# Kernel tuning notes

Hardware: AMD Instinct MI355X
Metric: run time of the kernel (lower is better)

The kernel has to match this reference:

```python
import jax, jax.numpy as jnp
import numpy as np

N = 8192
IN_C = 512
OUT_C = 512


def setup_inputs() -> dict:
    key = jax.random.key(0)
    k1, k2, k3 = jax.random.split(key, 3)
    x = jax.random.normal(k1, (N, IN_C), dtype=jnp.float32)
    adj = jax.random.uniform(k2, (N, N), dtype=jnp.float32)
    # torch.rand initializer for the weight (uniform [0,1))
    w = jax.random.uniform(k3, (IN_C, OUT_C), dtype=jnp.float32)
    return {"x": x, "adj": adj, "w": w}


def reference(x, adj, w):
    # A = adj + I
    A = adj + jnp.eye(adj.shape[0], dtype=adj.dtype)
    # D_hat = diag(deg)^{-1/2}; diagonal inverse + sqrt == elementwise rsqrt of degrees
    deg = jnp.sum(A, axis=1)                      # [N]
    d_inv_sqrt = jax.lax.rsqrt(deg)               # [N]
    # A_hat = D_hat @ A @ D_hat == row/col scaling (same math, no dense inverse)
    A_hat = A * d_inv_sqrt[:, None] * d_inv_sqrt[None, :]
    mm_1 = A_hat @ x                              # [N, in_c]
    return jax.nn.elu(mm_1 @ w)                   # [N, out_c]
```

## Files before the change

### kernel.cpp

```cpp
#include <hip/hip_runtime.h>

#define NN 8192
#define CC 512

typedef __attribute__((ext_vector_type(8))) short short8;
typedef __attribute__((ext_vector_type(4))) float f32x4;
typedef unsigned short ushort_t;

__device__ __forceinline__ unsigned short f2bf(float f) {
    unsigned int u = __float_as_uint(f);
    u += 0x7FFF + ((u >> 16) & 1);
    return (unsigned short)(u >> 16);
}
__device__ __forceinline__ float bf2f(unsigned short u) {
    return __uint_as_float(((unsigned int)u) << 16);
}

__device__ __forceinline__ void gload_lds16(const void* g, void* l) {
    __builtin_amdgcn_global_load_lds((const __attribute__((address_space(1))) unsigned int*)g,
                                     (__attribute__((address_space(3))) unsigned int*)l,
                                     16, 0, 0);
}

__global__ __launch_bounds__(256) void k_pre(const float* __restrict__ x,
                                             const float* __restrict__ adj,
                                             const ushort_t* __restrict__ wt,
                                             float* __restrict__ ds,
                                             ushort_t* __restrict__ adj16,
                                             float* __restrict__ z) {
    __shared__ __align__(16) ushort_t As[128 * 64];
    __shared__ __align__(16) ushort_t Bs[128 * 64];
    __shared__ float partial[4];

    int t = threadIdx.x;
    if (blockIdx.x >= 256) {
        int row = blockIdx.x - 256;
        const float4* p = (const float4*)(adj + (size_t)row * NN);
        ushort4* q = (ushort4*)(adj16 + (size_t)row * NN);
        float s = 0.f;
#pragma unroll
        for (int i = 0; i < 8; ++i) {
            float4 v = p[t + i * 256];
            s += (v.x + v.y) + (v.z + v.w);
            ushort4 u;
            u.x = f2bf(v.x); u.y = f2bf(v.y); u.z = f2bf(v.z); u.w = f2bf(v.w);
            q[t + i * 256] = u;
        }
#pragma unroll
        for (int off = 32; off > 0; off >>= 1) s += __shfl_down(s, off, 64);
        if ((t & 63) == 0) partial[t >> 6] = s;
        __syncthreads();
        if (t == 0) {
            float deg = ((partial[0] + partial[1]) + (partial[2] + partial[3])) + 1.0f;
            ds[row] = rsqrtf(deg);
        }
        return;
    }

    int bid = blockIdx.x;
    int wid = t >> 6, lane = t & 63;
    int cb = bid & 3, rb = bid >> 2;
    int rowBase = rb * 128, colBase = cb * 128;

    int ar = t >> 4, ac4 = t & 15;
    const float* aptr = x + (size_t)(rowBase + ar) * CC + ac4 * 4;
    int srow0 = t >> 3, ss = t & 7;

    f32x4 acc[4][4] = {};
    int wr = wid >> 1, wc = wid & 1;
    int fr = lane & 15, fq = lane >> 4;

    for (int kt = 0; kt < CC / 64; ++kt) {
#pragma unroll
        for (int i2 = 0; i2 < 8; ++i2) {
            float4 v = *(const float4*)(aptr + kt * 64 + (size_t)i2 * 16 * CC);
            int row = i2 * 16 + ar;
            ushort4 u2;
            u2.x = f2bf(v.x); u2.y = f2bf(v.y); u2.z = f2bf(v.z); u2.w = f2bf(v.w);
            *(ushort4*)((char*)As + row * 128 + ((ac4 * 8) ^ ((row & 7) << 4))) = u2;
        }
#pragma unroll
        for (int j = 0; j < 4; ++j) {
            int row = j * 32 + srow0;
            gload_lds16((const char*)(wt + (size_t)(colBase + row) * CC + kt * 64 +
                                      ((ss ^ (row & 7)) << 3)),
                        (char*)Bs + j * 4096 + wid * 1024);
        }
        __syncthreads();
#pragma unroll
        for (int ks = 0; ks < 2; ++ks) {
            short8 af[4], bfv[4];
#pragma unroll
            for (int m = 0; m < 4; ++m) {
                int row = wr * 64 + m * 16 + fr;
                af[m] = *(const short8*)((const char*)As + row * 128 +
                                         ((ks * 64 + fq * 16) ^ ((row & 7) << 4)));
            }
#pragma unroll
            for (int n = 0; n < 4; ++n) {
                int col = wc * 64 + n * 16 + fr;
                bfv[n] = *(const short8*)((const char*)Bs + col * 128 +
                                          ((ks * 64 + fq * 16) ^ ((col & 7) << 4)));
            }
#pragma unroll
            for (int m = 0; m < 4; ++m)
#pragma unroll
                for (int n = 0; n < 4; ++n)
                    acc[m][n] = __builtin_amdgcn_mfma_f32_16x16x32_bf16(af[m], bfv[n], acc[m][n], 0, 0, 0);
        }
        __syncthreads();
    }

#pragma unroll
    for (int m = 0; m < 4; ++m) {
#pragma unroll
        for (int j = 0; j < 4; ++j) {
            int gr = rowBase + wr * 64 + m * 16 + fq * 4 + j;
#pragma unroll
            for (int n = 0; n < 4; ++n) {
                int gc = colBase + wc * 64 + n * 16 + fr;
                z[(size_t)gr * CC + gc] = acc[m][n][j];
            }
        }
    }
}

__global__ __launch_bounds__(256) void k_rowsum(const float* __restrict__ adj,
                                                float* __restrict__ ds) {
    int row = blockIdx.x;
    const float4* p = (const float4*)(adj + (size_t)row * NN);
    float s = 0.f;
#pragma unroll
    for (int i = 0; i < 8; ++i) {
        float4 v = p[threadIdx.x + i * 256];
        s += (v.x + v.y) + (v.z + v.w);
    }
#pragma unroll
    for (int off = 32; off > 0; off >>= 1) s += __shfl_down(s, off, 64);
    __shared__ float partial[4];
    if ((threadIdx.x & 63) == 0) partial[threadIdx.x >> 6] = s;
    __syncthreads();
    if (threadIdx.x == 0) {
        float deg = ((partial[0] + partial[1]) + (partial[2] + partial[3])) + 1.0f;
        ds[row] = rsqrtf(deg);
    }
}

__global__ __launch_bounds__(256) void k_transpose(const float* __restrict__ in,
                                                   ushort_t* __restrict__ out,
                                                   const float* __restrict__ scale,
                                                   int R, int C) {
    __shared__ float tile[64][65];
    int r0 = blockIdx.x * 64, c0 = blockIdx.y * 64;
    int t = threadIdx.x;
    int cl = t & 63;
    int rl0 = t >> 6;
#pragma unroll
    for (int i = 0; i < 16; ++i) {
        int r = rl0 + i * 4;
        float v = in[(size_t)(r0 + r) * C + c0 + cl];
        float sc = scale ? scale[r0 + r] : 1.0f;
        tile[r][cl] = v * sc;
    }
    __syncthreads();
#pragma unroll
    for (int i = 0; i < 16; ++i) {
        int c = rl0 + i * 4;
        int r = cl;
        out[(size_t)(c0 + c) * R + r0 + r] = f2bf(tile[r][c]);
    }
}

template <bool ELU>
__global__ __launch_bounds__(256, 2) void k_gemm2t(const ushort_t* __restrict__ A,
                                                   const ushort_t* __restrict__ Bt,
                                                   float* __restrict__ out) {
    __shared__ __align__(16) ushort_t As[128 * 64];
    __shared__ __align__(16) ushort_t Bs[128 * 64];

    int t = threadIdx.x;
    int wid = t >> 6, lane = t & 63;
    int bid = blockIdx.x;
    bid = (bid & 7) * 32 + (bid >> 3);
    int cb = bid & 3, rb = bid >> 2;
    int rowBase = rb * 128, colBase = cb * 128;

    int srow0 = t >> 3, ss = t & 7;

    f32x4 acc[4][4] = {};
    int wr = wid >> 1, wc = wid & 1;
    int fr = lane & 15, fq = lane >> 4;

    for (int kt = 0; kt < CC / 64; ++kt) {
#pragma unroll
        for (int j = 0; j < 4; ++j) {
            int row = j * 32 + srow0;
            gload_lds16((const char*)(A + (size_t)(rowBase + row) * CC + kt * 64 +
                                      ((ss ^ (row & 7)) << 3)),
                        (char*)As + j * 4096 + wid * 1024);
            gload_lds16((const char*)(Bt + (size_t)(colBase + row) * CC + kt * 64 +
                                      ((ss ^ (row & 7)) << 3)),
                        (char*)Bs + j * 4096 + wid * 1024);
        }
        __syncthreads();
#pragma unroll
        for (int ks = 0; ks < 2; ++ks) {
            short8 af[4], bfv[4];
#pragma unroll
            for (int m = 0; m < 4; ++m) {
                int row = wr * 64 + m * 16 + fr;
                af[m] = *(const short8*)((const char*)As + row * 128 +
                                         ((ks * 64 + fq * 16) ^ ((row & 7) << 4)));
            }
#pragma unroll
            for (int n = 0; n < 4; ++n) {
                int col = wc * 64 + n * 16 + fr;
                bfv[n] = *(const short8*)((const char*)Bs + col * 128 +
                                          ((ks * 64 + fq * 16) ^ ((col & 7) << 4)));
            }
#pragma unroll
            for (int m = 0; m < 4; ++m)
#pragma unroll
                for (int n = 0; n < 4; ++n)
                    acc[m][n] = __builtin_amdgcn_mfma_f32_16x16x32_bf16(af[m], bfv[n], acc[m][n], 0, 0, 0);
        }
        __syncthreads();
    }

#pragma unroll
    for (int m = 0; m < 4; ++m) {
#pragma unroll
        for (int j = 0; j < 4; ++j) {
            int gr = rowBase + wr * 64 + m * 16 + fq * 4 + j;
#pragma unroll
            for (int n = 0; n < 4; ++n) {
                int gc = colBase + wc * 64 + n * 16 + fr;
                float v = acc[m][n][j];
                out[(size_t)gr * CC + gc] = ELU ? (v > 0.f ? v : expm1f(v)) : v;
            }
        }
    }
}

__global__ __launch_bounds__(512, 2) void k_gemm1d(const ushort_t* __restrict__ adj16,
                                                   const ushort_t* __restrict__ yt2,
                                                   ushort_t* __restrict__ part16) {
    __shared__ __align__(16) ushort_t Al[4][256 * 32];
    __shared__ __align__(16) ushort_t Bl[4][256 * 32];

    int t = threadIdx.x;
    int wid = t >> 6, lane = t & 63;
    int fr = lane & 15, fq = lane >> 4;

    int gid = blockIdx.x;
    int xcd = gid & 7, slot = gid >> 3;
    int cb = slot & 1;
    int u = (slot >> 1) + 16 * xcd;
    int rb = u & 31, ks = u >> 5;
    int rowBase = rb * 256, colBase = cb * 256;
    int kt0 = ks * 64;

    int wr = wid >> 2, wc = wid & 3;
    int bcol0 = (wc & 1) * 64;

    int srow = t >> 2;
    int sw = ((t & 3) ^ ((srow >> 1) & 3)) << 3;
    const ushort_t* aBase = adj16 + (size_t)(rowBase + srow) * NN + sw;
    const ushort_t* bBase = yt2 + (size_t)(colBase + srow) * NN + sw;

    auto stageA = [&](int buf, int tile) {
        gload_lds16(aBase + (size_t)tile * 32, (char*)Al[buf] + wid * 1024);
        gload_lds16(aBase + (size_t)128 * NN + (size_t)tile * 32, (char*)Al[buf] + 8192 + wid * 1024);
    };
    auto stageB = [&](int buf, int tile) {
        gload_lds16(bBase + (size_t)tile * 32, (char*)Bl[buf] + wid * 1024);
        gload_lds16(bBase + (size_t)128 * NN + (size_t)tile * 32, (char*)Bl[buf] + 8192 + wid * 1024);
    };

    f32x4 acc[8][4] = {};
    int sws = (fq ^ ((fr >> 1) & 3)) << 4;

    auto readA0 = [&](short8 (&d)[4], int buf) {
        const char* Ab = (const char*)Al[buf] + wr * 8192;
#pragma unroll
        for (int m = 0; m < 4; ++m) d[m] = *(const short8*)(Ab + (m * 16 + fr) * 64 + sws);
    };
    auto readA1 = [&](short8 (&d)[4], int buf) {
        const char* Ab = (const char*)Al[buf] + wr * 8192;
#pragma unroll
        for (int m = 0; m < 4; ++m) d[m] = *(const short8*)(Ab + (64 + m * 16 + fr) * 64 + sws);
    };
    auto readB = [&](short8 (&d)[4], int buf) {
        const char* Bb = (const char*)Bl[buf] + (wc >> 1) * 8192;
#pragma unroll
        for (int n = 0; n < 4; ++n) d[n] = *(const short8*)(Bb + (bcol0 + n * 16 + fr) * 64 + sws);
    };

    auto iter = [&](int i, short8 (&cf0)[4], short8 (&cbf)[4],
                    short8 (&nf0)[4], short8 (&nbf)[4]) {
        int nbuf = (i + 3) & 3;
        int ntile = kt0 + ((i + 3) & 63);
        short8 af1[4];
        readA1(af1, i & 3);
        stageA(nbuf, ntile);
        __builtin_amdgcn_s_barrier();
        __builtin_amdgcn_s_setprio(1);
#pragma unroll
        for (int m = 0; m < 4; ++m)
#pragma unroll
            for (int n = 0; n < 4; ++n)
                acc[m][n] = __builtin_amdgcn_mfma_f32_16x16x32_bf16(cf0[m], cbf[n], acc[m][n], 0, 0, 0);
        __builtin_amdgcn_s_setprio(0);
        __builtin_amdgcn_s_barrier();
        stageB(nbuf, ntile);
        asm volatile("s_waitcnt vmcnt(8)" ::: "memory");
        __builtin_amdgcn_sched_barrier(0);
        __builtin_amdgcn_s_barrier();
        readA0(nf0, (i + 1) & 3);
        readB(nbf, (i + 1) & 3);
        __builtin_amdgcn_s_setprio(1);
#pragma unroll
        for (int m = 0; m < 4; ++m)
#pragma unroll
            for (int n = 0; n < 4; ++n)
                acc[4 + m][n] = __builtin_amdgcn_mfma_f32_16x16x32_bf16(af1[m], cbf[n], acc[4 + m][n], 0, 0, 0);
        __builtin_amdgcn_s_setprio(0);
        __builtin_amdgcn_s_barrier();
    };

    stageA(0, kt0 + 0); stageB(0, kt0 + 0);
    stageA(1, kt0 + 1); stageB(1, kt0 + 1);
    stageA(2, kt0 + 2); stageB(2, kt0 + 2);
    asm volatile("s_waitcnt vmcnt(8)" ::: "memory");
    __builtin_amdgcn_sched_barrier(0);
    __builtin_amdgcn_s_barrier();

    short8 pf0[4], pbf[4], qf0[4], qbf[4];
    readA0(pf0, 0);
    readB(pbf, 0);

    for (int ii = 0; ii < 32; ++ii) {
        iter(2 * ii,     pf0, pbf, qf0, qbf);
        iter(2 * ii + 1, qf0, qbf, pf0, pbf);
    }

#pragma unroll
    for (int m = 0; m < 8; ++m) {
#pragma unroll
        for (int jj = 0; jj < 4; ++jj) {
            int gr = rowBase + wr * 128 + m * 16 + fq * 4 + jj;
            ushort_t* dst = part16 + ((size_t)ks * NN + gr) * CC + colBase;
#pragma unroll
            for (int n = 0; n < 4; ++n)
                dst[wc * 64 + n * 16 + fr] = f2bf(acc[m][n][jj]);
        }
    }
}

__global__ __launch_bounds__(256) void k_finish2(const ushort_t* __restrict__ part16,
                                                 const float* __restrict__ ds,
                                                 const float* __restrict__ z,
                                                 float* __restrict__ out) {
    size_t i = (size_t)blockIdx.x * 256 + threadIdx.x;
    const size_t stride = (size_t)NN * CC / 4;
    float s0 = 0.f, s1 = 0.f, s2 = 0.f, s3 = 0.f;
#pragma unroll
    for (int k = 0; k < 4; ++k) {
        ushort4 p = ((const ushort4*)part16)[i + k * stride];
        s0 += bf2f(p.x); s1 += bf2f(p.y); s2 += bf2f(p.z); s3 += bf2f(p.w);
    }
    int row = (int)(i >> 7);
    float d = ds[row];
    float d2 = d * d;
    f32x4 zv = ((const f32x4*)z)[i];
    f32x4 o;
    float v;
    v = d * s0 + d2 * zv[0]; o[0] = v > 0.f ? v : expm1f(v);
    v = d * s1 + d2 * zv[1]; o[1] = v > 0.f ? v : expm1f(v);
    v = d * s2 + d2 * zv[2]; o[2] = v > 0.f ? v : expm1f(v);
    v = d * s3 + d2 * zv[3]; o[3] = v > 0.f ? v : expm1f(v);
    ((f32x4*)out)[i] = o;
}

__global__ __launch_bounds__(256, 4) void k_gemm1_fb(const float* __restrict__ adj,
                                                     const ushort_t* __restrict__ yt,
                                                     const float* __restrict__ ds,
                                                     const float* __restrict__ x,
                                                     ushort_t* __restrict__ mm1) {
    __shared__ __align__(16) ushort_t As[128 * 64];
    __shared__ __align__(16) ushort_t Bs[128 * 64];

    int t = threadIdx.x;
    int wid = t >> 6, lane = t & 63;
    int bid = blockIdx.x;
    bid = (bid & 7) * 32 + (bid >> 3);
    int colBase = (bid & 3) * 128;
    int rowBase = (bid >> 2) * 128;

    int ar = t >> 4;
    int ac4 = t & 15;
    const float* aptr = adj + (size_t)(rowBase + ar) * NN + ac4 * 4;
    int brow0 = t >> 3;
    int bs = t & 7;
    float4 areg[8];

    auto loadA = [&](int kt) {
        const float* p = aptr + kt * 64;
#pragma unroll
        for (int i = 0; i < 8; ++i)
            areg[i] = *(const float4*)(p + (size_t)i * 16 * NN);
    };
    auto writeA = [&]() {
#pragma unroll
        for (int i = 0; i < 8; ++i) {
            int row = i * 16 + ar;
            ushort4 u;
            u.x = f2bf(areg[i].x); u.y = f2bf(areg[i].y);
            u.z = f2bf(areg[i].z); u.w = f2bf(areg[i].w);
            *(ushort4*)((char*)As + row * 128 + ((ac4 * 8) ^ ((row & 7) << 4))) = u;
        }
    };

    f32x4 acc[4][4] = {};
    int wr = wid >> 1, wc = wid & 1;
    int fr = lane & 15, fq = lane >> 4;

    loadA(0);
    for (int kt = 0; kt < NN / 64; ++kt) {
        writeA();
#pragma unroll
        for (int j = 0; j < 4; ++j) {
            int row = j * 32 + brow0;
            gload_lds16((const char*)(yt + (size_t)(colBase + row) * NN + kt * 64 +
                                      ((bs ^ (row & 7)) << 3)),
                        (char*)Bs + j * 4096 + wid * 1024);
        }
        __syncthreads();
        if (kt + 1 < NN / 64) loadA(kt + 1);
#pragma unroll
        for (int ks2 = 0; ks2 < 2; ++ks2) {
            short8 af[4], bfv[4];
#pragma unroll
            for (int m = 0; m < 4; ++m) {
                int row = wr * 64 + m * 16 + fr;
                af[m] = *(const short8*)((const char*)As + row * 128 +
                                         ((ks2 * 64 + fq * 16) ^ ((row & 7) << 4)));
            }
#pragma unroll
            for (int n = 0; n < 4; ++n) {
                int col = wc * 64 + n * 16 + fr;
                bfv[n] = *(const short8*)((const char*)Bs + col * 128 +
                                          ((ks2 * 64 + fq * 16) ^ ((col & 7) << 4)));
            }
#pragma unroll
            for (int m = 0; m < 4; ++m)
#pragma unroll
                for (int n = 0; n < 4; ++n)
                    acc[m][n] = __builtin_amdgcn_mfma_f32_16x16x32_bf16(af[m], bfv[n], acc[m][n], 0, 0, 0);
        }
        __syncthreads();
    }

#pragma unroll
    for (int m = 0; m < 4; ++m) {
#pragma unroll
        for (int j = 0; j < 4; ++j) {
            int gr = rowBase + wr * 64 + m * 16 + fq * 4 + j;
            float dsr = ds[gr];
#pragma unroll
            for (int n = 0; n < 4; ++n) {
                int gc = colBase + wc * 64 + n * 16 + fr;
                float v = dsr * (acc[m][n][j] + dsr * x[(size_t)gr * CC + gc]);
                mm1[(size_t)gr * CC + gc] = f2bf(v);
            }
        }
    }
}

extern "C" void kernel_launch(void* const* d_in, const int* in_sizes, int n_in,
                              void* d_out, int out_size, void* d_ws, size_t ws_size,
                              hipStream_t stream) {
    const float* x   = (const float*)d_in[0];
    const float* adj = (const float*)d_in[1];
    const float* w   = (const float*)d_in[2];
    float* out = (float*)d_out;

    char* ws = (char*)d_ws;
    size_t off = 0;
    float*    ds  = (float*)(ws + off);  off += 32u << 10;
    ushort_t* yt  = (ushort_t*)(ws + off);  off += 8u << 20;
    ushort_t* wt  = (ushort_t*)(ws + off);  off += 512u << 10;
    ushort_t* xb  = (ushort_t*)(ws + off);  off += 8u << 20;
    float*    z   = (float*)(ws + off);  off += 16u << 20;
    ushort_t* part16 = (ushort_t*)(ws + off);  off += 32u << 20;
    ushort_t* adj16  = (ushort_t*)(ws + off);
    const size_t adjBytes = (size_t)NN * NN * 2;

    if (ws_size >= off + adjBytes) {
        k_transpose<<<dim3(CC / 64, CC / 64), 256, 0, stream>>>(w, wt, nullptr, CC, CC);
        k_pre<<<NN + 256, 256, 0, stream>>>(x, adj, wt, ds, adj16, z);
        k_transpose<<<dim3(NN / 64, CC / 64), 256, 0, stream>>>(z, yt, ds, NN, CC);
        k_gemm1d<<<256, 512, 0, stream>>>(adj16, yt, part16);
        k_finish2<<<NN * CC / 4 / 256, 256, 0, stream>>>(part16, ds, z, out);
    } else {
        ushort_t* mm1 = xb;
        k_rowsum<<<NN, 256, 0, stream>>>(adj, ds);
        k_transpose<<<dim3(NN / 64, CC / 64), 256, 0, stream>>>(x, yt, ds, NN, CC);
        k_transpose<<<dim3(CC / 64, CC / 64), 256, 0, stream>>>(w, wt, nullptr, CC, CC);
        k_gemm1_fb<<<256, 256, 0, stream>>>(adj, yt, ds, x, mm1);
        k_gemm2t<true><<<256, 256, 0, stream>>>(mm1, wt, out);
    }
}
```

Measured before the change: 196.8 us.

## Shrink main GEMM tile to 256x128 and use simpler 3-stage pipeline

The bf16 adjacency GEMM now uses 256x128 output tiles instead of 256x256, launching 512 blocks instead of 256. Each wave holds a 64x64 accumulator instead of 128x64, and launch bounds ask for 4 blocks per CU. The 4-buffer split A0/A1 ping-pong schedule is replaced by a plain 3-buffer loop that loads fragments, prefetches two tiles ahead, runs the MFMAs and then waits. This trades higher occupancy and more blocks for lower arithmetic intensity: the adjacency matrix is now re-read four times instead of twice, and the finer schedule overlap is lost.

```diff
diff --git a/kernel.cpp b/kernel.cpp
--- a/kernel.cpp
+++ b/kernel.cpp
@@ -242,11 +242,11 @@
     }
 }
 
-__global__ __launch_bounds__(512, 2) void k_gemm1d(const ushort_t* __restrict__ adj16,
+__global__ __launch_bounds__(512, 4) void k_gemm1e(const ushort_t* __restrict__ adj16,
                                                    const ushort_t* __restrict__ yt2,
                                                    ushort_t* __restrict__ part16) {
-    __shared__ __align__(16) ushort_t Al[4][256 * 32];
-    __shared__ __align__(16) ushort_t Bl[4][256 * 32];
+    __shared__ __align__(16) ushort_t Al[3][256 * 32];
+    __shared__ __align__(16) ushort_t Bl[3][128 * 32];
 
     int t = threadIdx.x;
     int wid = t >> 6, lane = t & 63;
@@ -254,101 +254,69 @@
 
     int gid = blockIdx.x;
     int xcd = gid & 7, slot = gid >> 3;
-    int cb = slot & 1;
-    int u = (slot >> 1) + 16 * xcd;
-    int rb = u & 31, ks = u >> 5;
-    int rowBase = rb * 256, colBase = cb * 256;
+    int cb = slot & 3;
+    int v = (slot >> 2) + 16 * xcd;
+    int rb = v & 31, ks = v >> 5;
+    int rowBase = rb * 256, colBase = cb * 128;
     int kt0 = ks * 64;
 
-    int wr = wid >> 2, wc = wid & 3;
-    int bcol0 = (wc & 1) * 64;
-
+    int wr = wid >> 1, wc = wid & 1;
     int srow = t >> 2;
     int sw = ((t & 3) ^ ((srow >> 1) & 3)) << 3;
     const ushort_t* aBase = adj16 + (size_t)(rowBase + srow) * NN + sw;
     const ushort_t* bBase = yt2 + (size_t)(colBase + srow) * NN + sw;
 
-    auto stageA = [&](int buf, int tile) {
+    auto stage = [&](int buf, int tile) {
         gload_lds16(aBase + (size_t)tile * 32, (char*)Al[buf] + wid * 1024);
         gload_lds16(aBase + (size_t)128 * NN + (size_t)tile * 32, (char*)Al[buf] + 8192 + wid * 1024);
+        gload_lds16(bBase + (size_t)tile * 32, (char*)Bl[buf] + wid * 1024);
     };
-    auto stageB = [&](int buf, int tile) {
-        gload_lds16(bBase + (size_t)tile * 32, (char*)Bl[buf] + wid * 1024);
-        gload_lds16(bBase + (size_t)128 * NN + (size_t)tile * 32, (char*)Bl[buf] + 8192 + wid * 1024);
-    };
-
-    f32x4 acc[8][4] = {};
+
+    f32x4 acc[4][4] = {};
     int sws = (fq ^ ((fr >> 1) & 3)) << 4;
 
-    auto readA0 = [&](short8 (&d)[4], int buf) {
-        const char* Ab = (const char*)Al[buf] + wr * 8192;
-#pragma unroll
-        for (int m = 0; m < 4; ++m) d[m] = *(const short8*)(Ab + (m * 16 + fr) * 64 + sws);
-    };
-    auto readA1 = [&](short8 (&d)[4], int buf) {
-        const char* Ab = (const char*)Al[buf] + wr * 8192;
-#pragma unroll
-        for (int m = 0; m < 4; ++m) d[m] = *(const short8*)(Ab + (64 + m * 16 + fr) * 64 + sws);
-    };
-    auto readB = [&](short8 (&d)[4], int buf) {
-        const char* Bb = (const char*)Bl[buf] + (wc >> 1) * 8192;
-#pragma unroll
-        for (int n = 0; n < 4; ++n) d[n] = *(const short8*)(Bb + (bcol0 + n * 16 + fr) * 64 + sws);
-    };
-
-    auto iter = [&](int i, short8 (&cf0)[4], short8 (&cbf)[4],
-                    short8 (&nf0)[4], short8 (&nbf)[4]) {
-        int nbuf = (i + 3) & 3;
-        int ntile = kt0 + ((i + 3) & 63);
-        short8 af1[4];
-        readA1(af1, i & 3);
-        stageA(nbuf, ntile);
-        __builtin_amdgcn_s_barrier();
+    stage(0, kt0 + 0);
+    stage(1, kt0 + 1);
+    asm volatile("s_waitcnt vmcnt(3)" ::: "memory");
+    __builtin_amdgcn_sched_barrier(0);
+    __builtin_amdgcn_s_barrier();
+
+    int cur = 0, nxt = 2;
+    for (int i = 0; i < 64; ++i) {
+        const char* Ab = (const char*)Al[cur] + wr * 4096;
+        const char* Bb = (const char*)Bl[cur] + wc * 4096;
+
+        short8 af[4], bfv[4];
+#pragma unroll
+        for (int m = 0; m < 4; ++m)
+            af[m] = *(const short8*)(Ab + (m * 16 + fr) * 64 + sws);
+#pragma unroll
+        for (int n = 0; n < 4; ++n)
+            bfv[n] = *(const short8*)(Bb + (n * 16 + fr) * 64 + sws);
+
+        stage(nxt, kt0 + ((i + 2) & 63));
+
         __builtin_amdgcn_s_setprio(1);
 #pragma unroll
         for (int m = 0; m < 4; ++m)
 #pragma unroll
             for (int n = 0; n < 4; ++n)
-                acc[m][n] = __builtin_amdgcn_mfma_f32_16x16x32_bf16(cf0[m], cbf[n], acc[m][n], 0, 0, 0);
+                acc[m][n] = __builtin_amdgcn_mfma_f32_16x16x32_bf16(af[m], bfv[n], acc[m][n], 0, 0, 0);
         __builtin_amdgcn_s_setprio(0);
-        __builtin_amdgcn_s_barrier();
-        stageB(nbuf, ntile);
-        asm volatile("s_waitcnt vmcnt(8)" ::: "memory");
+
+        asm volatile("s_waitcnt vmcnt(3)" ::: "memory");
         __builtin_amdgcn_sched_barrier(0);
         __builtin_amdgcn_s_barrier();
-        readA0(nf0, (i + 1) & 3);
-        readB(nbf, (i + 1) & 3);
-        __builtin_amdgcn_s_setprio(1);
-#pragma unroll
-        for (int m = 0; m < 4; ++m)
-#pragma unroll
-            for (int n = 0; n < 4; ++n)
-                acc[4 + m][n] = __builtin_amdgcn_mfma_f32_16x16x32_bf16(af1[m], cbf[n], acc[4 + m][n], 0, 0, 0);
-        __builtin_amdgcn_s_setprio(0);
-        __builtin_amdgcn_s_barrier();
-    };
-
-    stageA(0, kt0 + 0); stageB(0, kt0 + 0);
-    stageA(1, kt0 + 1); stageB(1, kt0 + 1);
-    stageA(2, kt0 + 2); stageB(2, kt0 + 2);
-    asm volatile("s_waitcnt vmcnt(8)" ::: "memory");
-    __builtin_amdgcn_sched_barrier(0);
-    __builtin_amdgcn_s_barrier();
-
-    short8 pf0[4], pbf[4], qf0[4], qbf[4];
-    readA0(pf0, 0);
-    readB(pbf, 0);
-
-    for (int ii = 0; ii < 32; ++ii) {
-        iter(2 * ii,     pf0, pbf, qf0, qbf);
-        iter(2 * ii + 1, qf0, qbf, pf0, pbf);
-    }
-
-#pragma unroll
-    for (int m = 0; m < 8; ++m) {
+
+        cur = cur == 2 ? 0 : cur + 1;
+        nxt = nxt == 2 ? 0 : nxt + 1;
+    }
+
+#pragma unroll
+    for (int m = 0; m < 4; ++m) {
 #pragma unroll
         for (int jj = 0; jj < 4; ++jj) {
-            int gr = rowBase + wr * 128 + m * 16 + fq * 4 + jj;
+            int gr = rowBase + wr * 64 + m * 16 + fq * 4 + jj;
             ushort_t* dst = part16 + ((size_t)ks * NN + gr) * CC + colBase;
 #pragma unroll
             for (int n = 0; n < 4; ++n)
@@ -500,7 +468,7 @@
         k_transpose<<<dim3(CC / 64, CC / 64), 256, 0, stream>>>(w, wt, nullptr, CC, CC);
         k_pre<<<NN + 256, 256, 0, stream>>>(x, adj, wt, ds, adj16, z);
         k_transpose<<<dim3(NN / 64, CC / 64), 256, 0, stream>>>(z, yt, ds, NN, CC);
-        k_gemm1d<<<256, 512, 0, stream>>>(adj16, yt, part16);
+        k_gemm1e<<<512, 512, 0, stream>>>(adj16, yt, part16);
         k_finish2<<<NN * CC / 4 / 256, 256, 0, stream>>>(part16, ds, z, out);
     } else {
         ushort_t* mm1 = xb;
```

After: 195.7 us (median of 3 runs). Within noise of the previous version (-0.6%).
